# Performance work log

Hardware: AMD Instinct MI355X
Metric: run time of the kernel (lower is better)

The kernel has to match this reference:

```python
import jax, jax.numpy as jnp
import numpy as np

N_VOX = 500000
P, S, K = 2048, 64, 8          # pixels(rays), samples per ray, voxel neighbors per sample
F_M, F_H = 64, 128             # voxel feature dim, mlp hidden dim
FREQ_PE = 4
DEPTH_MIN, DEPTH_MAX = 1.0, 80.0
RAY_SAMPLE_STEPS = 64.0
EPS = 1e-10
IN_FEAT = F_M + 3 * FREQ_PE * 2  # 88


def lrelu(x):
    return jnp.where(x >= 0, x, 0.1 * x)  # LeakyReLU(0.1)


def posenc(x, L=FREQ_PE):
    # NeRF positional encoding: sin/cos(2^i * x), i in [0, L)
    freqs = 2.0 ** jnp.arange(L, dtype=x.dtype)          # [L]
    ang = x[..., None] * freqs                            # [..., 3, L]
    enc = jnp.concatenate([jnp.sin(ang), jnp.cos(ang)], axis=-1)  # [..., 3, 2L]
    return enc.reshape(x.shape[:-1] + (x.shape[-1] * 2 * L,))


def setup_inputs() -> dict:
    key = jax.random.key(0)
    ks = jax.random.split(key, 16)

    def xavier(k, fan_in, fan_out):
        return jax.random.normal(k, (fan_in, fan_out), jnp.float32) / np.sqrt(fan_in)

    inp = {
        'map_xyz': jax.random.normal(ks[0], (N_VOX, 3), jnp.float32),
        'map_feat': jax.random.normal(ks[1], (N_VOX, F_M), jnp.float32) * 0.05,
        'ind_voxel': jax.random.randint(ks[2], (P, S, K), 0, N_VOX),
        'sample_xyz': jax.random.normal(ks[3], (P, S, 3), jnp.float32),
        'dist_to_cam': jax.random.uniform(ks[4], (P, S), jnp.float32) * RAY_SAMPLE_STEPS,
        'W0': xavier(ks[5], IN_FEAT, F_H), 'b0': jnp.full((F_H,), 0.01, jnp.float32),
        'W1': xavier(ks[6], F_H, F_H),     'b1': jnp.full((F_H,), 0.01, jnp.float32),
        'W2': xavier(ks[7], F_H, F_H),     'b2': jnp.full((F_H,), 0.01, jnp.float32),
        'Wa0': xavier(ks[8], F_H, F_H // 2), 'ba0': jnp.full((F_H // 2,), 0.01, jnp.float32),
        'Wa1': xavier(ks[9], F_H // 2, 1),   'ba1': jnp.full((1,), 0.01, jnp.float32),
        'Wr0': xavier(ks[10], F_H, F_H // 2), 'br0': jnp.full((F_H // 2,), 0.01, jnp.float32),
        'Wr1': xavier(ks[11], F_H // 2, 3),   'br1': jnp.full((3,), 0.01, jnp.float32),
    }
    return inp


def reference(map_xyz, map_feat, ind_voxel, sample_xyz, dist_to_cam,
              W0, b0, W1, b1, W2, b2, Wa0, ba0, Wa1, ba1, Wr0, br0, Wr1, br1):
    # ---- voxel -> sample messages (func_msg_voxel_to_sample) ----
    voxel_xyz = map_xyz[ind_voxel]                       # [P,S,K,3] gather
    feat = map_feat[ind_voxel]                           # [P,S,K,F_M] gather
    offset = sample_xyz[:, :, None, :] - voxel_xyz       # [P,S,K,3]
    h = jnp.concatenate([feat, posenc(offset)], axis=-1) # [P,S,K,88]
    h = lrelu(h @ W0 + b0)
    h = lrelu(h @ W1 + b1)
    h = lrelu(h @ W2 + b2)                               # [P,S,K,F_H]
    w = jnp.exp(-10.0 * jnp.linalg.norm(offset, axis=-1))  # [P,S,K]
    w = w / jnp.sum(w, axis=-1, keepdims=True)
    # ---- reduce over K neighbors (func_reduce_voxel_to_sample) ----
    feat_s = jnp.sum(h * w[..., None], axis=2)           # [P,S,F_H]
    a = lrelu(feat_s @ Wa0 + ba0)
    alpha = jax.nn.sigmoid(a @ Wa1 + ba1)                # [P,S,1]
    r = lrelu(feat_s @ Wr0 + br0)
    rgb = jax.nn.sigmoid(r @ Wr1 + br1)                  # [P,S,3]
    # ---- sample -> pixel volume rendering (func_reduce_sample_to_pixel) ----
    dist = DEPTH_MIN + DEPTH_MAX * dist_to_cam / RAY_SAMPLE_STEPS  # [P,S]
    ones = jnp.ones((P, 1, 1), alpha.dtype)
    trans = jnp.cumprod(jnp.concatenate([ones, 1.0 - alpha + EPS], axis=1), axis=1)[:, :-1, :]
    blend = alpha * trans                                # [P,S,1]
    pixel_rgb = jnp.sum(rgb * blend, axis=1)             # [P,3]
    pixel_d = jnp.sum(dist[..., None] * blend, axis=1)   # [P,1]
    acc = jnp.sum(blend, axis=1)                         # [P,1]
    return jnp.concatenate([pixel_rgb, pixel_d, acc], axis=-1)  # [P,5]
```

## Files before the change

kernel.cpp:

```cpp
#include <hip/hip_runtime.h>

typedef __bf16 bf16_t;
typedef __bf16 bf16x4 __attribute__((ext_vector_type(4)));
typedef __bf16 bf16x8 __attribute__((ext_vector_type(8)));
typedef float  f32x4  __attribute__((ext_vector_type(4)));

#define NPIX 2048
#define NS   64
#define NK   8
#define NSAMP (NPIX*NS)
#define NROWS (NSAMP*NK)
#define TROWS 64
#define NTILES (NROWS/TROWS)
#define XSTR 104
#define HSTR 136

#define PK_W0 0
#define PK_W1 1536
#define PK_W2 3584
#define PK_WA 5632
#define PK_WR 6656
#define PK_TOT 7680

#define WS_AR_BYTES 122880

__global__ void pack_weights(const float* __restrict__ W0, const float* __restrict__ W1,
                             const float* __restrict__ W2, const float* __restrict__ Wa0,
                             const float* __restrict__ Wr0, bf16_t* __restrict__ dst0) {
  int tid = blockIdx.x * blockDim.x + threadIdx.x;
  if (tid >= PK_TOT * 8) return;
  const float* src; bf16_t* dst; int e, KD, ND, KS;
  if (tid < 12288)      { src = W0;  dst = dst0;         e = tid;         KD = 88;  ND = 128; KS = 3; }
  else if (tid < 28672) { src = W1;  dst = dst0 + 12288; e = tid - 12288; KD = 128; ND = 128; KS = 4; }
  else if (tid < 45056) { src = W2;  dst = dst0 + 28672; e = tid - 28672; KD = 128; ND = 128; KS = 4; }
  else if (tid < 53248) { src = Wa0; dst = dst0 + 45056; e = tid - 45056; KD = 128; ND = 64;  KS = 4; }
  else                  { src = Wr0; dst = dst0 + 53248; e = tid - 53248; KD = 128; ND = 64;  KS = 4; }
  int j = e & 7, l = (e >> 3) & 63, f = e >> 9;
  int s = f % KS, t = f / KS;
  int row = s * 32 + (l >> 4) * 8 + j;
  int col = t * 16 + (l & 15);
  float v = (row < KD) ? src[row * ND + col] : 0.f;
  dst[e] = (bf16_t)v;
}

__device__ __forceinline__ float lrelu(float v) { return fmaxf(v, 0.1f * v); }
__device__ __forceinline__ float sigmoidf(float x) { return 1.f / (1.f + __expf(-x)); }

__global__ __launch_bounds__(512, 4)
void nerf_main(const float* __restrict__ map_xyz, const float* __restrict__ map_feat,
               const int* __restrict__ ind, const float* __restrict__ sample_xyz,
               const float* __restrict__ b0g, const float* __restrict__ b1g,
               const float* __restrict__ b2g, const float* __restrict__ ba0g,
               const float* __restrict__ wa1g, const float* __restrict__ ba1g,
               const float* __restrict__ br0g, const float* __restrict__ wr1g,
               const float* __restrict__ br1g, const bf16_t* __restrict__ wpack,
               float* __restrict__ ar_out)
{
  __shared__ __align__(16) bf16_t sBuf[TROWS * HSTR];
  __shared__ __align__(16) bf16_t sHa[TROWS * HSTR];
  __shared__ __align__(16) bf16_t sFS[16 * HSTR];
  __shared__ __align__(16) float sWt[TROWS];
  __shared__ float sWs[8];
  __shared__ float sA[8 * 68];
  __shared__ float sR[8 * 68];
  __shared__ float sWa1[64];
  __shared__ float sWr1[192];

  const int tid = threadIdx.x;
  const int wid = tid >> 6, l = tid & 63;
  const int q = l >> 4, n = l & 15;

  const bf16x8* pk = (const bf16x8*)wpack;
  bf16x8 w0f[3], w1f[4], w2f[4], hdf[4];
#pragma unroll
  for (int s = 0; s < 3; s++) w0f[s] = pk[PK_W0 + (wid * 3 + s) * 64 + l];
#pragma unroll
  for (int s = 0; s < 4; s++) w1f[s] = pk[PK_W1 + (wid * 4 + s) * 64 + l];
#pragma unroll
  for (int s = 0; s < 4; s++) w2f[s] = pk[PK_W2 + (wid * 4 + s) * 64 + l];
#pragma unroll
  for (int s = 0; s < 4; s++)
    hdf[s] = pk[(wid < 4 ? PK_WA : PK_WR) + ((wid & 3) * 4 + s) * 64 + l];

  const int col = wid * 16 + n;
  const float bias0 = b0g[col], bias1 = b1g[col], bias2 = b2g[col];
  const float biasH = (wid < 4) ? ba0g[(wid & 3) * 16 + n] : br0g[(wid & 3) * 16 + n];

  if (tid < 64) sWa1[tid] = wa1g[tid];
  else if (tid < 256) sWr1[tid - 64] = wr1g[tid - 64];
  for (int i = tid; i < 8 * HSTR; i += 512) sFS[8 * HSTR + i] = (bf16_t)0.f;
  const float ba1v = ba1g[0];
  const float br1v0 = br1g[0], br1v1 = br1g[1], br1v2 = br1g[2];
  __syncthreads();

  for (int tile = blockIdx.x; tile < NTILES; tile += gridDim.x) {
    const int m0 = tile * TROWS;

    {
      const int r = tid >> 3, p = tid & 7;
      const int m = m0 + r;
      const int idx = ind[m];
      const float4* fp = (const float4*)(map_feat + (size_t)idx * 64 + p * 8);
      float4 f0 = fp[0], f1 = fp[1];
      bf16x8 v;
      v[0] = (bf16_t)f0.x; v[1] = (bf16_t)f0.y; v[2] = (bf16_t)f0.z; v[3] = (bf16_t)f0.w;
      v[4] = (bf16_t)f1.x; v[5] = (bf16_t)f1.y; v[6] = (bf16_t)f1.z; v[7] = (bf16_t)f1.w;
      *(bf16x8*)(sBuf + r * XSTR + p * 8) = v;
      const int g = m >> 3;
      if (p < 6) {
        const int d = p >> 1;
        float o = sample_xyz[g * 3 + d] - map_xyz[idx * 3 + d];
        float s1 = __sinf(o), c1 = __cosf(o);
        float s2 = 2.f * s1 * c1, c2 = 1.f - 2.f * s1 * s1;
        float s4 = 2.f * s2 * c2, c4 = 1.f - 2.f * s2 * s2;
        float s8 = 2.f * s4 * c4, c8 = 1.f - 2.f * s4 * s4;
        bf16x4 e;
        if (p & 1) { e[0] = (bf16_t)c1; e[1] = (bf16_t)c2; e[2] = (bf16_t)c4; e[3] = (bf16_t)c8; }
        else       { e[0] = (bf16_t)s1; e[1] = (bf16_t)s2; e[2] = (bf16_t)s4; e[3] = (bf16_t)s8; }
        *(bf16x4*)(sBuf + r * XSTR + 64 + d * 8 + (p & 1) * 4) = e;
      } else if (p == 6) {
        bf16x8 z = {};
        *(bf16x8*)(sBuf + r * XSTR + 88) = z;
      } else {
        float ox = sample_xyz[g * 3 + 0] - map_xyz[idx * 3 + 0];
        float oy = sample_xyz[g * 3 + 1] - map_xyz[idx * 3 + 1];
        float oz = sample_xyz[g * 3 + 2] - map_xyz[idx * 3 + 2];
        sWt[r] = __expf(-10.f * sqrtf(ox * ox + oy * oy + oz * oz));
      }
    }
    __syncthreads();

    if (tid < 8) {
      float ss = 0.f;
#pragma unroll
      for (int k = 0; k < 8; k++) ss += sWt[tid * 8 + k];
      sWs[tid] = ss;
    }

    {
      f32x4 acc[4] = {};
#pragma unroll
      for (int s = 0; s < 3; s++)
#pragma unroll
        for (int g = 0; g < 4; g++) {
          bf16x8 a = *(const bf16x8*)(sBuf + (g * 16 + n) * XSTR + s * 32 + q * 8);
          acc[g] = __builtin_amdgcn_mfma_f32_16x16x32_bf16(a, w0f[s], acc[g], 0, 0, 0);
        }
#pragma unroll
      for (int g = 0; g < 4; g++)
#pragma unroll
        for (int i = 0; i < 4; i++) {
          float v = lrelu(acc[g][i] + bias0);
          sHa[(g * 16 + q * 4 + i) * HSTR + col] = (bf16_t)v;
        }
    }
    __syncthreads();

    {
      f32x4 acc[4] = {};
#pragma unroll
      for (int s = 0; s < 4; s++)
#pragma unroll
        for (int g = 0; g < 4; g++) {
          bf16x8 a = *(const bf16x8*)(sHa + (g * 16 + n) * HSTR + s * 32 + q * 8);
          acc[g] = __builtin_amdgcn_mfma_f32_16x16x32_bf16(a, w1f[s], acc[g], 0, 0, 0);
        }
#pragma unroll
      for (int g = 0; g < 4; g++)
#pragma unroll
        for (int i = 0; i < 4; i++) {
          float v = lrelu(acc[g][i] + bias1);
          sBuf[(g * 16 + q * 4 + i) * HSTR + col] = (bf16_t)v;
        }
    }
    __syncthreads();

    {
      f32x4 acc[4] = {};
#pragma unroll
      for (int s = 0; s < 4; s++)
#pragma unroll
        for (int g = 0; g < 4; g++) {
          bf16x8 a = *(const bf16x8*)(sBuf + (g * 16 + n) * HSTR + s * 32 + q * 8);
          acc[g] = __builtin_amdgcn_mfma_f32_16x16x32_bf16(a, w2f[s], acc[g], 0, 0, 0);
        }
#pragma unroll
      for (int g = 0; g < 4; g++) {
        const int j = 2 * g + (q >> 1);
        const float4 wt4 = *(const float4*)(sWt + j * 8 + 4 * (q & 1));
        float part = 0.f;
#pragma unroll
        for (int i = 0; i < 4; i++) {
          float v = lrelu(acc[g][i] + bias2);
          part += ((const float*)&wt4)[i] * v;
        }
        part += __shfl_xor(part, 16);
        float fs = part * __builtin_amdgcn_rcpf(sWs[j]);
        if (!(q & 1)) sFS[j * HSTR + col] = (bf16_t)fs;
      }
    }
    __syncthreads();

    {
      f32x4 ha = {};
#pragma unroll
      for (int s = 0; s < 4; s++) {
        bf16x8 a = *(const bf16x8*)(sFS + n * HSTR + s * 32 + q * 8);
        ha = __builtin_amdgcn_mfma_f32_16x16x32_bf16(a, hdf[s], ha, 0, 0, 0);
      }
      if (q < 2) {
        float* dst = (wid < 4) ? sA : sR;
#pragma unroll
        for (int i = 0; i < 4; i++) {
          float v = lrelu(ha[i] + biasH);
          dst[(q * 4 + i) * 68 + (wid & 3) * 16 + n] = v;
        }
      }
    }
    __syncthreads();

    {
      float vA = sA[wid * 68 + l];
      float vR = sR[wid * 68 + l];
      float xa = vA * sWa1[l];
      float x0 = vR * sWr1[l * 3 + 0];
      float x1 = vR * sWr1[l * 3 + 1];
      float x2 = vR * sWr1[l * 3 + 2];
#pragma unroll
      for (int d = 32; d > 0; d >>= 1) {
        xa += __shfl_xor(xa, d);
        x0 += __shfl_xor(x0, d);
        x1 += __shfl_xor(x1, d);
        x2 += __shfl_xor(x2, d);
      }
      if (l == 0) {
        float4 o;
        o.x = sigmoidf(x0 + br1v0);
        o.y = sigmoidf(x1 + br1v1);
        o.z = sigmoidf(x2 + br1v2);
        o.w = sigmoidf(xa + ba1v);
        ((float4*)ar_out)[m0 / 8 + wid] = o;
      }
    }
  }
}

__global__ __launch_bounds__(512)
void render_kernel(const float* __restrict__ ar, const float* __restrict__ dcam,
                   float* __restrict__ out) {
  int ray = blockIdx.x * 8 + (threadIdx.x >> 6);
  int s = threadIdx.x & 63;
  float4 v = ((const float4*)ar)[ray * 64 + s];
  float alpha = v.w;
  float t = 1.f - alpha + 1e-10f;
  float p = t;
#pragma unroll
  for (int d = 1; d < 64; d <<= 1) {
    float o = __shfl_up(p, d);
    if (s >= d) p *= o;
  }
  float pm1 = __shfl_up(p, 1);
  float T = (s == 0) ? 1.f : pm1;
  float bl = alpha * T;
  float dist = 1.f + 1.25f * dcam[ray * 64 + s];
  float cr = v.x * bl, cg = v.y * bl, cb = v.z * bl, cd = dist * bl, ca = bl;
#pragma unroll
  for (int d = 32; d > 0; d >>= 1) {
    cr += __shfl_xor(cr, d);
    cg += __shfl_xor(cg, d);
    cb += __shfl_xor(cb, d);
    cd += __shfl_xor(cd, d);
    ca += __shfl_xor(ca, d);
  }
  if (s == 0) {
    out[ray * 5 + 0] = cr; out[ray * 5 + 1] = cg; out[ray * 5 + 2] = cb;
    out[ray * 5 + 3] = cd; out[ray * 5 + 4] = ca;
  }
}

extern "C" void kernel_launch(void* const* d_in, const int* in_sizes, int n_in,
                              void* d_out, int out_size, void* d_ws, size_t ws_size,
                              hipStream_t stream) {
  const float* map_xyz    = (const float*)d_in[0];
  const float* map_feat   = (const float*)d_in[1];
  const int*   ind        = (const int*)d_in[2];
  const float* sample_xyz = (const float*)d_in[3];
  const float* dist_cam   = (const float*)d_in[4];
  const float* W0  = (const float*)d_in[5];
  const float* b0  = (const float*)d_in[6];
  const float* W1  = (const float*)d_in[7];
  const float* b1  = (const float*)d_in[8];
  const float* W2  = (const float*)d_in[9];
  const float* b2  = (const float*)d_in[10];
  const float* Wa0 = (const float*)d_in[11];
  const float* ba0 = (const float*)d_in[12];
  const float* Wa1 = (const float*)d_in[13];
  const float* ba1 = (const float*)d_in[14];
  const float* Wr0 = (const float*)d_in[15];
  const float* br0 = (const float*)d_in[16];
  const float* Wr1 = (const float*)d_in[17];
  const float* br1 = (const float*)d_in[18];

  bf16_t* wpack = (bf16_t*)d_ws;
  float*  ar    = (float*)((char*)d_ws + WS_AR_BYTES);

  pack_weights<<<240, 256, 0, stream>>>(W0, W1, W2, Wa0, Wr0, wpack);
  nerf_main<<<512, 512, 0, stream>>>(map_xyz, map_feat, ind, sample_xyz,
                                     b0, b1, b2, ba0, Wa1, ba1, br0, Wr1, br1,
                                     wpack, ar);
  render_kernel<<<256, 512, 0, stream>>>(ar, dist_cam, (float*)d_out);
}
```

Before: 417.1 us.

## Re-tile MLP MFMAs as 2x2 per wave and fold final heads into one MFMA

```diff
diff --git a/kernel.cpp b/kernel.cpp
--- a/kernel.cpp
+++ b/kernel.cpp
@@ -59,42 +59,67 @@
   __shared__ __align__(16) bf16_t sBuf[TROWS * HSTR];
   __shared__ __align__(16) bf16_t sHa[TROWS * HSTR];
   __shared__ __align__(16) bf16_t sFS[16 * HSTR];
+  __shared__ __align__(16) bf16_t sAR[16 * HSTR];
+  __shared__ __align__(16) bf16_t sFB[2048];
   __shared__ __align__(16) float sWt[TROWS];
   __shared__ float sWs[8];
-  __shared__ float sA[8 * 68];
-  __shared__ float sR[8 * 68];
-  __shared__ float sWa1[64];
-  __shared__ float sWr1[192];
 
   const int tid = threadIdx.x;
   const int wid = tid >> 6, l = tid & 63;
   const int q = l >> 4, n = l & 15;
+  const int cp = wid & 3, rh = wid >> 2;
 
   const bf16x8* pk = (const bf16x8*)wpack;
-  bf16x8 w0f[3], w1f[4], w2f[4], hdf[4];
-#pragma unroll
-  for (int s = 0; s < 3; s++) w0f[s] = pk[PK_W0 + (wid * 3 + s) * 64 + l];
-#pragma unroll
-  for (int s = 0; s < 4; s++) w1f[s] = pk[PK_W1 + (wid * 4 + s) * 64 + l];
-#pragma unroll
-  for (int s = 0; s < 4; s++) w2f[s] = pk[PK_W2 + (wid * 4 + s) * 64 + l];
-#pragma unroll
-  for (int s = 0; s < 4; s++)
-    hdf[s] = pk[(wid < 4 ? PK_WA : PK_WR) + ((wid & 3) * 4 + s) * 64 + l];
-
-  const int col = wid * 16 + n;
-  const float bias0 = b0g[col], bias1 = b1g[col], bias2 = b2g[col];
-  const float biasH = (wid < 4) ? ba0g[(wid & 3) * 16 + n] : br0g[(wid & 3) * 16 + n];
-
-  if (tid < 64) sWa1[tid] = wa1g[tid];
-  else if (tid < 256) sWr1[tid - 64] = wr1g[tid - 64];
-  for (int i = tid; i < 8 * HSTR; i += 512) sFS[8 * HSTR + i] = (bf16_t)0.f;
+  bf16x8 w1f[2][4], w2f[2][4];
+#pragma unroll
+  for (int nt = 0; nt < 2; nt++) {
+    int t = cp * 2 + nt;
+#pragma unroll
+    for (int s = 0; s < 4; s++) w1f[nt][s] = pk[PK_W1 + (t * 4 + s) * 64 + l];
+#pragma unroll
+    for (int s = 0; s < 4; s++) w2f[nt][s] = pk[PK_W2 + (t * 4 + s) * 64 + l];
+  }
+
+  float bias0[2], bias1[2], bias2[2];
+#pragma unroll
+  for (int nt = 0; nt < 2; nt++) {
+    int c = (cp * 2 + nt) * 16 + n;
+    bias0[nt] = b0g[c]; bias1[nt] = b1g[c]; bias2[nt] = b2g[c];
+  }
+  const float biasH = (wid < 4) ? ba0g[cp * 16 + n] : br0g[cp * 16 + n];
   const float ba1v = ba1g[0];
   const float br1v0 = br1g[0], br1v1 = br1g[1], br1v2 = br1g[2];
+
+  for (int i = tid; i < 8 * HSTR; i += 512) {
+    sFS[8 * HSTR + i] = (bf16_t)0.f;
+    sAR[8 * HSTR + i] = (bf16_t)0.f;
+  }
+  {
+    int e0 = tid * 4;
+    int jh = e0 & 7, ll = (e0 >> 3) & 63, s = e0 >> 9;
+#pragma unroll
+    for (int ii = 0; ii < 4; ii++) {
+      int j = jh + ii;
+      int k = s * 32 + (ll >> 4) * 8 + j;
+      int cc = ll & 15;
+      float v = 0.f;
+      if (cc < 3 && k < 64) v = wr1g[k * 3 + cc];
+      else if (cc == 3 && k >= 64) v = wa1g[k - 64];
+      sFB[e0 + ii] = (bf16_t)v;
+    }
+  }
   __syncthreads();
 
   for (int tile = blockIdx.x; tile < NTILES; tile += gridDim.x) {
     const int m0 = tile * TROWS;
+    const bf16x8* pkt = pk + (tile >> 20);
+
+    bf16x8 w0f[2][3];
+#pragma unroll
+    for (int nt = 0; nt < 2; nt++)
+#pragma unroll
+      for (int s = 0; s < 3; s++)
+        w0f[nt][s] = pkt[PK_W0 + ((cp * 2 + nt) * 3 + s) * 64 + l];
 
     {
       const int r = tid >> 3, p = tid & 7;
@@ -138,65 +163,86 @@
     }
 
     {
-      f32x4 acc[4] = {};
-#pragma unroll
-      for (int s = 0; s < 3; s++)
-#pragma unroll
-        for (int g = 0; g < 4; g++) {
-          bf16x8 a = *(const bf16x8*)(sBuf + (g * 16 + n) * XSTR + s * 32 + q * 8);
-          acc[g] = __builtin_amdgcn_mfma_f32_16x16x32_bf16(a, w0f[s], acc[g], 0, 0, 0);
-        }
-#pragma unroll
-      for (int g = 0; g < 4; g++)
-#pragma unroll
-        for (int i = 0; i < 4; i++) {
-          float v = lrelu(acc[g][i] + bias0);
-          sHa[(g * 16 + q * 4 + i) * HSTR + col] = (bf16_t)v;
-        }
-    }
-    __syncthreads();
-
-    {
-      f32x4 acc[4] = {};
-#pragma unroll
-      for (int s = 0; s < 4; s++)
-#pragma unroll
-        for (int g = 0; g < 4; g++) {
-          bf16x8 a = *(const bf16x8*)(sHa + (g * 16 + n) * HSTR + s * 32 + q * 8);
-          acc[g] = __builtin_amdgcn_mfma_f32_16x16x32_bf16(a, w1f[s], acc[g], 0, 0, 0);
-        }
-#pragma unroll
-      for (int g = 0; g < 4; g++)
-#pragma unroll
-        for (int i = 0; i < 4; i++) {
-          float v = lrelu(acc[g][i] + bias1);
-          sBuf[(g * 16 + q * 4 + i) * HSTR + col] = (bf16_t)v;
-        }
-    }
-    __syncthreads();
-
-    {
-      f32x4 acc[4] = {};
-#pragma unroll
-      for (int s = 0; s < 4; s++)
-#pragma unroll
-        for (int g = 0; g < 4; g++) {
-          bf16x8 a = *(const bf16x8*)(sBuf + (g * 16 + n) * HSTR + s * 32 + q * 8);
-          acc[g] = __builtin_amdgcn_mfma_f32_16x16x32_bf16(a, w2f[s], acc[g], 0, 0, 0);
-        }
-#pragma unroll
-      for (int g = 0; g < 4; g++) {
-        const int j = 2 * g + (q >> 1);
+      f32x4 acc[2][2] = {};
+#pragma unroll
+      for (int g = 0; g < 2; g++) {
+        const bf16_t* xb = sBuf + ((rh * 2 + g) * 16 + n) * XSTR + q * 8;
+#pragma unroll
+        for (int s = 0; s < 3; s++) {
+          bf16x8 a = *(const bf16x8*)(xb + s * 32);
+          acc[g][0] = __builtin_amdgcn_mfma_f32_16x16x32_bf16(a, w0f[0][s], acc[g][0], 0, 0, 0);
+          acc[g][1] = __builtin_amdgcn_mfma_f32_16x16x32_bf16(a, w0f[1][s], acc[g][1], 0, 0, 0);
+        }
+      }
+#pragma unroll
+      for (int g = 0; g < 2; g++)
+#pragma unroll
+        for (int nt = 0; nt < 2; nt++)
+#pragma unroll
+          for (int i = 0; i < 4; i++) {
+            float v = lrelu(acc[g][nt][i] + bias0[nt]);
+            sHa[((rh * 2 + g) * 16 + q * 4 + i) * HSTR + (cp * 2 + nt) * 16 + n] = (bf16_t)v;
+          }
+    }
+    __syncthreads();
+
+    {
+      f32x4 acc[2][2] = {};
+#pragma unroll
+      for (int g = 0; g < 2; g++) {
+        const bf16_t* hb = sHa + ((rh * 2 + g) * 16 + n) * HSTR + q * 8;
+#pragma unroll
+        for (int s = 0; s < 4; s++) {
+          bf16x8 a = *(const bf16x8*)(hb + s * 32);
+          acc[g][0] = __builtin_amdgcn_mfma_f32_16x16x32_bf16(a, w1f[0][s], acc[g][0], 0, 0, 0);
+          acc[g][1] = __builtin_amdgcn_mfma_f32_16x16x32_bf16(a, w1f[1][s], acc[g][1], 0, 0, 0);
+        }
+      }
+#pragma unroll
+      for (int g = 0; g < 2; g++)
+#pragma unroll
+        for (int nt = 0; nt < 2; nt++)
+#pragma unroll
+          for (int i = 0; i < 4; i++) {
+            float v = lrelu(acc[g][nt][i] + bias1[nt]);
+            sBuf[((rh * 2 + g) * 16 + q * 4 + i) * HSTR + (cp * 2 + nt) * 16 + n] = (bf16_t)v;
+          }
+    }
+    __syncthreads();
+
+    bf16x8 hdf[4];
+#pragma unroll
+    for (int s = 0; s < 4; s++)
+      hdf[s] = pkt[(wid < 4 ? PK_WA : PK_WR) + ((wid & 3) * 4 + s) * 64 + l];
+
+    {
+      f32x4 acc[2][2] = {};
+#pragma unroll
+      for (int g = 0; g < 2; g++) {
+        const bf16_t* hb = sBuf + ((rh * 2 + g) * 16 + n) * HSTR + q * 8;
+#pragma unroll
+        for (int s = 0; s < 4; s++) {
+          bf16x8 a = *(const bf16x8*)(hb + s * 32);
+          acc[g][0] = __builtin_amdgcn_mfma_f32_16x16x32_bf16(a, w2f[0][s], acc[g][0], 0, 0, 0);
+          acc[g][1] = __builtin_amdgcn_mfma_f32_16x16x32_bf16(a, w2f[1][s], acc[g][1], 0, 0, 0);
+        }
+      }
+#pragma unroll
+      for (int g = 0; g < 2; g++) {
+        const int j = rh * 4 + g * 2 + (q >> 1);
         const float4 wt4 = *(const float4*)(sWt + j * 8 + 4 * (q & 1));
-        float part = 0.f;
-#pragma unroll
-        for (int i = 0; i < 4; i++) {
-          float v = lrelu(acc[g][i] + bias2);
-          part += ((const float*)&wt4)[i] * v;
-        }
-        part += __shfl_xor(part, 16);
-        float fs = part * __builtin_amdgcn_rcpf(sWs[j]);
-        if (!(q & 1)) sFS[j * HSTR + col] = (bf16_t)fs;
+        const float inv = __builtin_amdgcn_rcpf(sWs[j]);
+#pragma unroll
+        for (int nt = 0; nt < 2; nt++) {
+          float part = 0.f;
+#pragma unroll
+          for (int i = 0; i < 4; i++) {
+            float v = lrelu(acc[g][nt][i] + bias2[nt]);
+            part += ((const float*)&wt4)[i] * v;
+          }
+          part += __shfl_xor(part, 16);
+          if (!(q & 1)) sFS[j * HSTR + (cp * 2 + nt) * 16 + n] = (bf16_t)(part * inv);
+        }
       }
     }
     __syncthreads();
@@ -209,37 +255,29 @@
         ha = __builtin_amdgcn_mfma_f32_16x16x32_bf16(a, hdf[s], ha, 0, 0, 0);
       }
       if (q < 2) {
-        float* dst = (wid < 4) ? sA : sR;
+        const int base = (wid < 4) ? 64 : 0;
 #pragma unroll
         for (int i = 0; i < 4; i++) {
           float v = lrelu(ha[i] + biasH);
-          dst[(q * 4 + i) * 68 + (wid & 3) * 16 + n] = v;
-        }
-      }
-    }
-    __syncthreads();
-
-    {
-      float vA = sA[wid * 68 + l];
-      float vR = sR[wid * 68 + l];
-      float xa = vA * sWa1[l];
-      float x0 = vR * sWr1[l * 3 + 0];
-      float x1 = vR * sWr1[l * 3 + 1];
-      float x2 = vR * sWr1[l * 3 + 2];
-#pragma unroll
-      for (int d = 32; d > 0; d >>= 1) {
-        xa += __shfl_xor(xa, d);
-        x0 += __shfl_xor(x0, d);
-        x1 += __shfl_xor(x1, d);
-        x2 += __shfl_xor(x2, d);
-      }
-      if (l == 0) {
-        float4 o;
-        o.x = sigmoidf(x0 + br1v0);
-        o.y = sigmoidf(x1 + br1v1);
-        o.z = sigmoidf(x2 + br1v2);
-        o.w = sigmoidf(xa + ba1v);
-        ((float4*)ar_out)[m0 / 8 + wid] = o;
+          sAR[(q * 4 + i) * HSTR + base + (wid & 3) * 16 + n] = (bf16_t)v;
+        }
+      }
+    }
+    __syncthreads();
+
+    if (wid == 0) {
+      f32x4 c = {};
+#pragma unroll
+      for (int s = 0; s < 4; s++) {
+        bf16x8 a = *(const bf16x8*)(sAR + n * HSTR + s * 32 + q * 8);
+        bf16x8 b = *(const bf16x8*)(sFB + (s * 64 + l) * 8);
+        c = __builtin_amdgcn_mfma_f32_16x16x32_bf16(a, b, c, 0, 0, 0);
+      }
+      if (q < 2 && n < 4) {
+        float bias = (n == 3) ? ba1v : ((n == 0) ? br1v0 : (n == 1) ? br1v1 : br1v2);
+#pragma unroll
+        for (int i = 0; i < 4; i++)
+          ar_out[(size_t)(m0 / 8 + q * 4 + i) * 4 + n] = sigmoidf(c[i] + bias);
       }
     }
   }
```

Result: slower. 499.9 us (+19.8%).

## Transpose MFMA operands, vectorize epilogue stores, and run final head as MFMA

Applied to the files above, without the earlier changes.

```diff
diff --git a/kernel.cpp b/kernel.cpp
--- a/kernel.cpp
+++ b/kernel.cpp
@@ -59,12 +59,10 @@
   __shared__ __align__(16) bf16_t sBuf[TROWS * HSTR];
   __shared__ __align__(16) bf16_t sHa[TROWS * HSTR];
   __shared__ __align__(16) bf16_t sFS[16 * HSTR];
+  __shared__ __align__(16) bf16_t sAR[16 * HSTR];
+  __shared__ __align__(16) bf16_t sFB[2048];
   __shared__ __align__(16) float sWt[TROWS];
   __shared__ float sWs[8];
-  __shared__ float sA[8 * 68];
-  __shared__ float sR[8 * 68];
-  __shared__ float sWa1[64];
-  __shared__ float sWr1[192];
 
   const int tid = threadIdx.x;
   const int wid = tid >> 6, l = tid & 63;
@@ -82,15 +80,29 @@
   for (int s = 0; s < 4; s++)
     hdf[s] = pk[(wid < 4 ? PK_WA : PK_WR) + ((wid & 3) * 4 + s) * 64 + l];
 
-  const int col = wid * 16 + n;
-  const float bias0 = b0g[col], bias1 = b1g[col], bias2 = b2g[col];
-  const float biasH = (wid < 4) ? ba0g[(wid & 3) * 16 + n] : br0g[(wid & 3) * 16 + n];
-
-  if (tid < 64) sWa1[tid] = wa1g[tid];
-  else if (tid < 256) sWr1[tid - 64] = wr1g[tid - 64];
-  for (int i = tid; i < 8 * HSTR; i += 512) sFS[8 * HSTR + i] = (bf16_t)0.f;
-  const float ba1v = ba1g[0];
-  const float br1v0 = br1g[0], br1v1 = br1g[1], br1v2 = br1g[2];
+  const float4 b0v = *(const float4*)(b0g + wid * 16 + q * 4);
+  const float4 b1v = *(const float4*)(b1g + wid * 16 + q * 4);
+  const float4 b2v = *(const float4*)(b2g + wid * 16 + q * 4);
+  const float4 bHv = *(const float4*)((wid < 4 ? ba0g : br0g) + (wid & 3) * 16 + q * 4);
+  float4 fbv; fbv.x = br1g[0]; fbv.y = br1g[1]; fbv.z = br1g[2]; fbv.w = ba1g[0];
+
+  for (int i = tid; i < 8 * HSTR; i += 512) {
+    sFS[8 * HSTR + i] = (bf16_t)0.f;
+    sAR[8 * HSTR + i] = (bf16_t)0.f;
+  }
+  {
+    int e0 = tid * 4;
+    int jb = e0 & 7, ll = (e0 >> 3) & 63, s = e0 >> 9;
+    int m = ll & 15;
+#pragma unroll
+    for (int ii = 0; ii < 4; ii++) {
+      int k = s * 32 + (ll >> 4) * 8 + jb + ii;
+      float v = 0.f;
+      if (k < 64)  { if (m < 3) v = wr1g[k * 3 + m]; }
+      else         { if (m == 3) v = wa1g[k - 64]; }
+      sFB[e0 + ii] = (bf16_t)v;
+    }
+  }
   __syncthreads();
 
   for (int tile = blockIdx.x; tile < NTILES; tile += gridDim.x) {
@@ -140,64 +152,80 @@
     {
       f32x4 acc[4] = {};
 #pragma unroll
-      for (int s = 0; s < 3; s++)
-#pragma unroll
-        for (int g = 0; g < 4; g++) {
-          bf16x8 a = *(const bf16x8*)(sBuf + (g * 16 + n) * XSTR + s * 32 + q * 8);
-          acc[g] = __builtin_amdgcn_mfma_f32_16x16x32_bf16(a, w0f[s], acc[g], 0, 0, 0);
+      for (int st = 0; st < 4; st++)
+#pragma unroll
+        for (int s = 0; s < 3; s++) {
+          bf16x8 b = *(const bf16x8*)(sBuf + (st * 16 + n) * XSTR + s * 32 + q * 8);
+          acc[st] = __builtin_amdgcn_mfma_f32_16x16x32_bf16(w0f[s], b, acc[st], 0, 0, 0);
         }
 #pragma unroll
-      for (int g = 0; g < 4; g++)
-#pragma unroll
-        for (int i = 0; i < 4; i++) {
-          float v = lrelu(acc[g][i] + bias0);
-          sHa[(g * 16 + q * 4 + i) * HSTR + col] = (bf16_t)v;
+      for (int st = 0; st < 4; st++) {
+        bf16x4 o;
+        o[0] = (bf16_t)lrelu(acc[st][0] + b0v.x);
+        o[1] = (bf16_t)lrelu(acc[st][1] + b0v.y);
+        o[2] = (bf16_t)lrelu(acc[st][2] + b0v.z);
+        o[3] = (bf16_t)lrelu(acc[st][3] + b0v.w);
+        *(bf16x4*)(sHa + (st * 16 + n) * HSTR + wid * 16 + q * 4) = o;
+      }
+    }
+    __syncthreads();
+
+    {
+      f32x4 acc[4] = {};
+#pragma unroll
+      for (int st = 0; st < 4; st++)
+#pragma unroll
+        for (int s = 0; s < 4; s++) {
+          bf16x8 b = *(const bf16x8*)(sHa + (st * 16 + n) * HSTR + s * 32 + q * 8);
+          acc[st] = __builtin_amdgcn_mfma_f32_16x16x32_bf16(w1f[s], b, acc[st], 0, 0, 0);
         }
+#pragma unroll
+      for (int st = 0; st < 4; st++) {
+        bf16x4 o;
+        o[0] = (bf16_t)lrelu(acc[st][0] + b1v.x);
+        o[1] = (bf16_t)lrelu(acc[st][1] + b1v.y);
+        o[2] = (bf16_t)lrelu(acc[st][2] + b1v.z);
+        o[3] = (bf16_t)lrelu(acc[st][3] + b1v.w);
+        *(bf16x4*)(sBuf + (st * 16 + n) * HSTR + wid * 16 + q * 4) = o;
+      }
     }
     __syncthreads();
 
     {
       f32x4 acc[4] = {};
 #pragma unroll
-      for (int s = 0; s < 4; s++)
-#pragma unroll
-        for (int g = 0; g < 4; g++) {
-          bf16x8 a = *(const bf16x8*)(sHa + (g * 16 + n) * HSTR + s * 32 + q * 8);
-          acc[g] = __builtin_amdgcn_mfma_f32_16x16x32_bf16(a, w1f[s], acc[g], 0, 0, 0);
+      for (int st = 0; st < 4; st++)
+#pragma unroll
+        for (int s = 0; s < 4; s++) {
+          bf16x8 b = *(const bf16x8*)(sBuf + (st * 16 + n) * HSTR + s * 32 + q * 8);
+          acc[st] = __builtin_amdgcn_mfma_f32_16x16x32_bf16(w2f[s], b, acc[st], 0, 0, 0);
         }
 #pragma unroll
-      for (int g = 0; g < 4; g++)
-#pragma unroll
-        for (int i = 0; i < 4; i++) {
-          float v = lrelu(acc[g][i] + bias1);
-          sBuf[(g * 16 + q * 4 + i) * HSTR + col] = (bf16_t)v;
-        }
-    }
-    __syncthreads();
-
-    {
-      f32x4 acc[4] = {};
-#pragma unroll
-      for (int s = 0; s < 4; s++)
-#pragma unroll
-        for (int g = 0; g < 4; g++) {
-          bf16x8 a = *(const bf16x8*)(sBuf + (g * 16 + n) * HSTR + s * 32 + q * 8);
-          acc[g] = __builtin_amdgcn_mfma_f32_16x16x32_bf16(a, w2f[s], acc[g], 0, 0, 0);
-        }
-#pragma unroll
-      for (int g = 0; g < 4; g++) {
-        const int j = 2 * g + (q >> 1);
-        const float4 wt4 = *(const float4*)(sWt + j * 8 + 4 * (q & 1));
-        float part = 0.f;
-#pragma unroll
-        for (int i = 0; i < 4; i++) {
-          float v = lrelu(acc[g][i] + bias2);
-          part += ((const float*)&wt4)[i] * v;
-        }
-        part += __shfl_xor(part, 16);
-        float fs = part * __builtin_amdgcn_rcpf(sWs[j]);
-        if (!(q & 1)) sFS[j * HSTR + col] = (bf16_t)fs;
-      }
+      for (int st = 0; st < 4; st++) {
+        bf16x4 o;
+        o[0] = (bf16_t)lrelu(acc[st][0] + b2v.x);
+        o[1] = (bf16_t)lrelu(acc[st][1] + b2v.y);
+        o[2] = (bf16_t)lrelu(acc[st][2] + b2v.z);
+        o[3] = (bf16_t)lrelu(acc[st][3] + b2v.w);
+        *(bf16x4*)(sHa + (st * 16 + n) * HSTR + wid * 16 + q * 4) = o;
+      }
+    }
+    __syncthreads();
+
+    {
+      int g = tid >> 6;
+      int c = (tid & 63) * 2;
+      float a0 = 0.f, a1 = 0.f;
+#pragma unroll
+      for (int k = 0; k < 8; k++) {
+        float wk = sWt[g * 8 + k];
+        unsigned u = *(const unsigned*)(sHa + (g * 8 + k) * HSTR + c);
+        a0 += wk * __uint_as_float(u << 16);
+        a1 += wk * __uint_as_float(u & 0xffff0000u);
+      }
+      float inv = 1.f / sWs[g];
+      sFS[g * HSTR + c]     = (bf16_t)(a0 * inv);
+      sFS[g * HSTR + c + 1] = (bf16_t)(a1 * inv);
     }
     __syncthreads();
 
@@ -205,41 +233,36 @@
       f32x4 ha = {};
 #pragma unroll
       for (int s = 0; s < 4; s++) {
-        bf16x8 a = *(const bf16x8*)(sFS + n * HSTR + s * 32 + q * 8);
-        ha = __builtin_amdgcn_mfma_f32_16x16x32_bf16(a, hdf[s], ha, 0, 0, 0);
-      }
-      if (q < 2) {
-        float* dst = (wid < 4) ? sA : sR;
-#pragma unroll
-        for (int i = 0; i < 4; i++) {
-          float v = lrelu(ha[i] + biasH);
-          dst[(q * 4 + i) * 68 + (wid & 3) * 16 + n] = v;
-        }
-      }
-    }
-    __syncthreads();
-
-    {
-      float vA = sA[wid * 68 + l];
-      float vR = sR[wid * 68 + l];
-      float xa = vA * sWa1[l];
-      float x0 = vR * sWr1[l * 3 + 0];
-      float x1 = vR * sWr1[l * 3 + 1];
-      float x2 = vR * sWr1[l * 3 + 2];
-#pragma unroll
-      for (int d = 32; d > 0; d >>= 1) {
-        xa += __shfl_xor(xa, d);
-        x0 += __shfl_xor(x0, d);
-        x1 += __shfl_xor(x1, d);
-        x2 += __shfl_xor(x2, d);
-      }
-      if (l == 0) {
+        bf16x8 b = *(const bf16x8*)(sFS + n * HSTR + s * 32 + q * 8);
+        ha = __builtin_amdgcn_mfma_f32_16x16x32_bf16(hdf[s], b, ha, 0, 0, 0);
+      }
+      if (n < 8) {
+        const int base = (wid < 4) ? 64 : 0;
+        bf16x4 o;
+        o[0] = (bf16_t)lrelu(ha[0] + bHv.x);
+        o[1] = (bf16_t)lrelu(ha[1] + bHv.y);
+        o[2] = (bf16_t)lrelu(ha[2] + bHv.z);
+        o[3] = (bf16_t)lrelu(ha[3] + bHv.w);
+        *(bf16x4*)(sAR + n * HSTR + base + (wid & 3) * 16 + q * 4) = o;
+      }
+    }
+    __syncthreads();
+
+    if (wid == 0) {
+      f32x4 c = {};
+#pragma unroll
+      for (int s = 0; s < 4; s++) {
+        bf16x8 a = *(const bf16x8*)(sFB + (s * 64 + l) * 8);
+        bf16x8 b = *(const bf16x8*)(sAR + n * HSTR + s * 32 + q * 8);
+        c = __builtin_amdgcn_mfma_f32_16x16x32_bf16(a, b, c, 0, 0, 0);
+      }
+      if (q == 0 && n < 8) {
         float4 o;
-        o.x = sigmoidf(x0 + br1v0);
-        o.y = sigmoidf(x1 + br1v1);
-        o.z = sigmoidf(x2 + br1v2);
-        o.w = sigmoidf(xa + ba1v);
-        ((float4*)ar_out)[m0 / 8 + wid] = o;
+        o.x = sigmoidf(c[0] + fbv.x);
+        o.y = sigmoidf(c[1] + fbv.y);
+        o.z = sigmoidf(c[2] + fbv.z);
+        o.w = sigmoidf(c[3] + fbv.w);
+        ((float4*)ar_out)[m0 / 8 + n] = o;
       }
     }
   }
```

Result: faster. 401.4 us (-3.8%).
